# Kernel optimization log

Measured on AMD Instinct MI355X. Metric: run time of the kernel, lower is better.

## Reference

```python
import jax, jax.numpy as jnp
import numpy as np

OBS_LEN = 16; PRED_LEN = 25; N = 192; P = N * N; GH = GW = 8
IN_DIM = 2; OUT_DIM = 5; ENC = 64; DEC = 128
EMB = 32; DYN = 32; C1 = 64; C2 = 16; SOC = 3 * 3 * C2

def lrelu(x):
    return jnp.where(x >= 0, x, 0.1 * x)

def lstm_step(x, h, c, Wih, Whh, bih, bhh):
    # torch nn.LSTM gate order: i, f, g, o
    z = x @ Wih.T + h @ Whh.T + (bih + bhh)
    i, f, g, o = jnp.split(z, 4, axis=-1)
    c = jax.nn.sigmoid(f) * c + jax.nn.sigmoid(i) * jnp.tanh(g)
    h = jax.nn.sigmoid(o) * jnp.tanh(c)
    return h, c

def _indexed_lstm(frames, idxs, n_states, Wip, bip, Wih, Whh, bih, bhh):
    # per-frame gather of hidden/cell rows -> one LSTM step -> scatter back
    H0 = jnp.zeros((n_states, ENC), jnp.float32)
    C0 = jnp.zeros((n_states, ENC), jnp.float32)
    def step(carry, inp):
        Hs, Cs = carry
        frame, idx = inp
        h, c = Hs[idx], Cs[idx]                       # gather [M, ENC]
        emb = lrelu(frame @ Wip.T + bip)              # [M, EMB]
        h, c = lstm_step(emb, h, c, Wih, Whh, bih, bhh)
        return (Hs.at[idx].set(h), Cs.at[idx].set(c)), None  # scatter
    (Hs, _), _ = jax.lax.scan(step, (H0, C0), (frames, idxs))
    return Hs

def setup_inputs():
    key = jax.random.key(0)
    ks = jax.random.split(key, 16)
    def w(k, shape, fan):
        return (jax.random.normal(k, shape, jnp.float32) / np.sqrt(fan)).astype(jnp.float32)
    inp = {}
    inp['obs_traj'] = jax.random.normal(ks[0], (OBS_LEN, N, IN_DIM), jnp.float32)
    inp['obs_ngbrs_traj'] = jax.random.normal(ks[1], (OBS_LEN, P, IN_DIM), jnp.float32)
    inp['masks'] = jnp.ones((N, GH, GW, ENC), dtype=bool)  # fully occupied social grid
    inp['masks_idxs'] = jax.random.randint(ks[2], (N * GH * GW,), 0, P)
    inp['obs_traj_idxs'] = jnp.tile(jnp.arange(N), (OBS_LEN, 1))        # all nodes present each frame
    inp['obs_ngbrs_traj_idxs'] = jnp.tile(jnp.arange(P), (OBS_LEN, 1))  # all pair slots present
    inp['num_nodes'] = N
    inp['Wip'] = w(ks[3], (EMB, IN_DIM), IN_DIM); inp['bip'] = jnp.zeros((EMB,), jnp.float32)
    inp['Wih_e'] = w(ks[4], (4 * ENC, EMB), EMB); inp['Whh_e'] = w(ks[5], (4 * ENC, ENC), ENC)
    inp['bih_e'] = jnp.zeros((4 * ENC,), jnp.float32); inp['bhh_e'] = jnp.zeros((4 * ENC,), jnp.float32)
    inp['Wdyn'] = w(ks[6], (DYN, ENC), ENC); inp['bdyn'] = jnp.zeros((DYN,), jnp.float32)
    inp['Wc1'] = w(ks[7], (C1, ENC, 3, 3), ENC * 9); inp['bc1'] = jnp.zeros((C1,), jnp.float32)
    inp['Wc2'] = w(ks[8], (C2, C1, 3, 3), C1 * 9); inp['bc2'] = jnp.zeros((C2,), jnp.float32)
    inp['Wih_d'] = w(ks[9], (4 * DEC, SOC + DYN), SOC + DYN); inp['Whh_d'] = w(ks[10], (4 * DEC, DEC), DEC)
    inp['bih_d'] = jnp.zeros((4 * DEC,), jnp.float32); inp['bhh_d'] = jnp.zeros((4 * DEC,), jnp.float32)
    inp['Wop'] = w(ks[11], (OUT_DIM, DEC), DEC); inp['bop'] = jnp.zeros((OUT_DIM,), jnp.float32)
    return inp

def reference(obs_traj, obs_ngbrs_traj, masks, masks_idxs, obs_traj_idxs,
              obs_ngbrs_traj_idxs, num_nodes, Wip, bip, Wih_e, Whh_e, bih_e, bhh_e,
              Wdyn, bdyn, Wc1, bc1, Wc2, bc2, Wih_d, Whh_d, bih_d, bhh_d, Wop, bop):
    B = obs_traj_idxs.shape[1]
    # ego-trajectory encoder: per-frame indexed LSTM over num_nodes state slots
    Hs = _indexed_lstm(obs_traj, obs_traj_idxs, num_nodes, Wip, bip, Wih_e, Whh_e, bih_e, bhh_e)
    final_h = Hs[obs_traj_idxs[-1]]                   # [B, ENC]
    traj_enc = lrelu(final_h @ Wdyn.T + bdyn)         # [B, DYN]
    # neighbor-pair encoder: per-frame indexed LSTM over num_nodes^2 state slots
    Hn = _indexed_lstm(obs_ngbrs_traj, obs_ngbrs_traj_idxs, num_nodes * num_nodes,
                       Wip, bip, Wih_e, Whh_e, bih_e, bhh_e)
    ngbr_h = Hn[masks_idxs]                           # [B*GH*GW, ENC]
    # masked_scatter_ of neighbor encodings into fully-occupied social grid == reshape
    soc = jnp.where(masks, ngbr_h.reshape(B, GH, GW, ENC), 0.0)
    soc = jnp.transpose(soc, (0, 3, 2, 1))            # [B, ENC, GW, GH]
    dn = ('NCHW', 'OIHW', 'NCHW')
    soc = lrelu(jax.lax.conv_general_dilated(soc, Wc1, (1, 1), 'VALID', dimension_numbers=dn)
                + bc1[None, :, None, None])           # [B, C1, 6, 6]
    soc = lrelu(jax.lax.conv_general_dilated(soc, Wc2, (1, 1), 'VALID', dimension_numbers=dn)
                + bc2[None, :, None, None])           # [B, C2, 4, 4]
    soc = jax.lax.reduce_window(soc, -jnp.inf, jax.lax.max, (1, 1, 2, 2), (1, 1, 1, 1), 'VALID')
    soc = soc.reshape(B, SOC)                         # [B, 144]
    enc = jnp.concatenate([traj_enc, soc], axis=1)    # [B, DYN+SOC]
    h0 = jnp.zeros((B, DEC), jnp.float32); c0 = jnp.zeros((B, DEC), jnp.float32)
    def dec_step(carry, _):
        h, c = carry
        h, c = lstm_step(enc, h, c, Wih_d, Whh_d, bih_d, bhh_d)
        return (h, c), h
    _, hs = jax.lax.scan(dec_step, (h0, c0), None, length=PRED_LEN)
    o = hs @ Wop.T + bop                              # [PRED_LEN, B, 5]
    # bivariate Gaussian output activation (mu_x, mu_y, sigma_x, sigma_y, corr)
    return jnp.stack([o[..., 0], o[..., 1], jnp.exp(o[..., 2]),
                      jnp.exp(o[..., 3]), jnp.tanh(o[..., 4])], axis=-1)
```

## Files before the change

kernel.cpp:

```cpp
#include <hip/hip_runtime.h>
#include <hip/hip_bf16.h>

#define OBS_LEN 16
#define PRED_LEN 25
#define NNODES 192
#define PAIRS 36864
#define ENC 64
#define EMB 32
#define KTOT 96
#define DEC 128
#define SOCDYN 176
#define PAIR_GROUPS 2304
#define EGO_GROUPS 12

typedef short short8 __attribute__((ext_vector_type(8)));
typedef float f32x4 __attribute__((ext_vector_type(4)));

__device__ __forceinline__ float sigm(float x) {
    return __builtin_amdgcn_rcpf(1.f + __expf(-x));
}
__device__ __forceinline__ float tanh_f(float x) {
    return fmaf(-2.f, __builtin_amdgcn_rcpf(1.f + __expf(2.f * x)), 1.f);
}
__device__ __forceinline__ float lrelu(float x) { return (x >= 0.f) ? x : 0.1f * x; }

__device__ __forceinline__ unsigned short f2bf(float f) {
    union { float f; unsigned u; } v; v.f = f;
    unsigned r = v.u + 0x7fffu + ((v.u >> 16) & 1u);
    return (unsigned short)(r >> 16);
}
__device__ __forceinline__ float bf2f(unsigned short s) {
    union { unsigned u; float f; } v; v.u = ((unsigned)s) << 16; return v.f;
}

__global__ __launch_bounds__(1024, 1)
void prep_dedup_kernel(const float* __restrict__ Wih_d, const float* __restrict__ Whh_d,
                       const float* __restrict__ Wc1, const float* __restrict__ Wc2,
                       const int* __restrict__ masks_idxs,
                       unsigned short* __restrict__ Whh_bf, unsigned short* __restrict__ Wih_bf,
                       float* __restrict__ WT1, float* __restrict__ WT2,
                       int* __restrict__ list, int* __restrict__ list_count)
{
    const int t = threadIdx.x, b = blockIdx.x;
    if (b < 205) {
        int idx = b * 1024 + t;
        if (idx < 65536) {
            int m = idx >> 7, k = idx & 127;
            Whh_bf[idx] = f2bf(Whh_d[m * 128 + k]);
        } else if (idx < 65536 + 98304) {
            int i = idx - 65536;
            int m = i / 192, k = i % 192;
            Wih_bf[i] = (k < 176) ? f2bf(Wih_d[m * 176 + k]) : (unsigned short)0;
        } else if (idx < 65536 + 98304 + 36864) {
            int i = idx - (65536 + 98304);
            int s = i >> 6, o = i & 63;
            int c = s / 9, tap = s % 9;
            WT1[i] = Wc1[(o * 64 + c) * 9 + tap];
        } else {
            int i = idx - (65536 + 98304 + 36864);
            int s = i >> 4, o = i & 15;
            int c = s / 9, tap = s % 9;
            WT2[i] = Wc2[(o * 64 + c) * 9 + tap];
        }
        return;
    }
    __shared__ unsigned bm[1152];
    __shared__ int pcs[1024];
    for (int i = t; i < 1152; i += 1024) bm[i] = 0u;
    __syncthreads();
    for (int i = t; i < 12288; i += 1024) {
        const int r = masks_idxs[i];
        atomicOr(&bm[r >> 5], 1u << (r & 31));
    }
    __syncthreads();
    int pc = 0;
    if (t < 576) pc = __popc(bm[2 * t]) + __popc(bm[2 * t + 1]);
    pcs[t] = pc;
    __syncthreads();
    for (int ofs = 1; ofs < 1024; ofs <<= 1) {
        int v = (t >= ofs) ? pcs[t - ofs] : 0;
        __syncthreads();
        pcs[t] += v;
        __syncthreads();
    }
    if (t == 1023) list_count[0] = pcs[1023];
    if (t < 576) {
        int base = pcs[t] - pc;
#pragma unroll
        for (int wi = 0; wi < 2; ++wi) {
            unsigned wv = bm[2 * t + wi];
            const int rowbase = (2 * t + wi) * 32;
            while (wv) {
                const int bit = __ffs(wv) - 1;
                list[base++] = rowbase + bit;
                wv &= wv - 1;
            }
        }
    }
}

__global__ __launch_bounds__(256, 3)
void enc_lstm_kernel(const float* __restrict__ obs_traj,
                     const float* __restrict__ obs_ngbrs,
                     const float* __restrict__ Wip, const float* __restrict__ bip,
                     const float* __restrict__ Wih, const float* __restrict__ Whh,
                     const float* __restrict__ bih, const float* __restrict__ bhh,
                     const int* __restrict__ list, const int* __restrict__ list_count,
                     float* __restrict__ Hn,
                     float* __restrict__ final_h)
{
    __shared__ __align__(16) short embs[16 * 16 * 40];
    __shared__ __align__(16) short hb[2][16 * 72];
    __shared__ int rows_s[16];

    const int t = threadIdx.x;
    const int wj = t >> 6, lane = t & 63, ln = lane & 15, kq = lane >> 4;
    const int b = blockIdx.x;
    const bool is_ego = (b >= PAIR_GROUPS);

    if (!is_ego) {
        const int cnt = list_count[0];
        if (b * 16 >= cnt) return;
        if (t < 16) rows_s[t] = list[min(b * 16 + t, cnt - 1)];
    } else {
        if (t < 16) rows_s[t] = (b - PAIR_GROUPS) * 16 + t;
    }

    short8 afrag[4][3];
#pragma unroll
    for (int g = 0; g < 4; ++g)
#pragma unroll
        for (int kc = 0; kc < 3; ++kc) {
            const int m = g * 64 + wj * 16 + ln;
            const float* wp = (kc == 0) ? (Wih + m * 32 + kq * 8)
                                        : (Whh + m * 64 + (kc - 1) * 32 + kq * 8);
            short8 a;
#pragma unroll
            for (int j = 0; j < 8; ++j) a[j] = (short)f2bf(wp[j]);
            afrag[g][kc] = a;
        }

    float bsv[4][4];
#pragma unroll
    for (int g = 0; g < 4; ++g)
#pragma unroll
        for (int r = 0; r < 4; ++r) {
            const int m = g * 64 + wj * 16 + kq * 4 + r;
            bsv[g][r] = bih[m] + bhh[m];
        }

    __syncthreads();

    {
        const int row = t & 15, stp = t >> 4;
        const int r = rows_s[row];
        const float* sp = is_ego ? (obs_traj + stp * NNODES * 2)
                                 : (obs_ngbrs + stp * PAIRS * 2);
        const float x0 = sp[r * 2 + 0];
        const float x1 = sp[r * 2 + 1];
        unsigned* dst = (unsigned*)&embs[(stp * 16 + row) * 40];
#pragma unroll
        for (int k = 0; k < 32; k += 2) {
            const float e0 = lrelu(fmaf(x0, Wip[2 * k + 0], fmaf(x1, Wip[2 * k + 1], bip[k])));
            const float e1 = lrelu(fmaf(x0, Wip[2 * k + 2], fmaf(x1, Wip[2 * k + 3], bip[k + 1])));
            dst[k >> 1] = (unsigned)f2bf(e0) | ((unsigned)f2bf(e1) << 16);
        }
    }
    for (int i = t; i < 2 * 16 * 72 / 2; i += 256) ((unsigned*)hb)[i] = 0u;
    __syncthreads();

    float cst[4] = {0.f, 0.f, 0.f, 0.f};
    int p = 0;
    for (int stp = 0; stp < OBS_LEN; ++stp) {
        const short8 bf0 = *(const short8*)&embs[(stp * 16 + ln) * 40 + kq * 8];
        const short* hbp = &hb[p][ln * 72 + kq * 8];
        const short8 bf1 = *(const short8*)hbp;
        const short8 bf2 = *(const short8*)(hbp + 32);
        f32x4 acc[4];
#pragma unroll
        for (int g = 0; g < 4; ++g) {
            f32x4 a = { bsv[g][0], bsv[g][1], bsv[g][2], bsv[g][3] };
            a = __builtin_amdgcn_mfma_f32_16x16x32_bf16(afrag[g][0], bf0, a, 0, 0, 0);
            a = __builtin_amdgcn_mfma_f32_16x16x32_bf16(afrag[g][1], bf1, a, 0, 0, 0);
            acc[g] = __builtin_amdgcn_mfma_f32_16x16x32_bf16(afrag[g][2], bf2, a, 0, 0, 0);
        }
        unsigned long long pk = 0;
#pragma unroll
        for (int r = 0; r < 4; ++r) {
            const float cn = fmaf(sigm(acc[1][r]), cst[r], sigm(acc[0][r]) * tanh_f(acc[2][r]));
            cst[r] = cn;
            const float h = sigm(acc[3][r]) * tanh_f(cn);
            pk |= (unsigned long long)f2bf(h) << (16 * r);
        }
        __syncthreads();
        *(unsigned long long*)&hb[1 - p][ln * 72 + wj * 16 + kq * 4] = pk;
        p ^= 1;
        __syncthreads();
    }

    {
        const int row = t >> 4, k0 = (t & 15) * 4;
        unsigned long long pk = *(const unsigned long long*)&hb[p][row * 72 + k0];
        float4 v;
        v.x = bf2f((unsigned short)(pk));
        v.y = bf2f((unsigned short)(pk >> 16));
        v.z = bf2f((unsigned short)(pk >> 32));
        v.w = bf2f((unsigned short)(pk >> 48));
        float* dst = is_ego ? (final_h + rows_s[row] * 64 + k0)
                            : (Hn + (long)rows_s[row] * 64 + k0);
        *(float4*)dst = v;
    }
}

__global__ __launch_bounds__(256, 2)
void conv_kernel(const float* __restrict__ Hn, const int* __restrict__ masks_idxs,
                 const float* __restrict__ final_h, const float* __restrict__ Wdyn,
                 const float* __restrict__ bdyn, const float* __restrict__ WT1,
                 const float* __restrict__ bc1, const float* __restrict__ WT2,
                 const float* __restrict__ bc2, float* __restrict__ enc)
{
    __shared__ float in2[64][66];
    __shared__ float s1[64 * 37];
    __shared__ float s2[16 * 17];
    const int t = threadIdx.x, b = blockIdx.x;

    for (int i = 0; i < 16; ++i) {
        const int c = t & 63;
        const int p = (i << 2) + (t >> 6);
        const int u = p >> 3, v = p & 7;
        const int row = masks_idxs[b * 64 + v * 8 + u];
        in2[c][p] = Hn[(long)row * 64 + c];
    }
    if (t < 32) {
        float acc = bdyn[t];
        for (int k = 0; k < 64; ++k) acc = fmaf(final_h[b * 64 + k], Wdyn[t * 64 + k], acc);
        enc[b * SOCDYN + t] = lrelu(acc);
    }
    __syncthreads();

    {
        const int wv = t >> 6, o = t & 63;
        const int xb = (wv >> 1) * 3, yb = (wv & 1) * 3;
        float a1[3][3];
        const float bc = bc1[o];
#pragma unroll
        for (int qx = 0; qx < 3; ++qx)
#pragma unroll
            for (int qy = 0; qy < 3; ++qy) a1[qx][qy] = bc;
        for (int c = 0; c < 64; ++c) {
            float win[5][5];
#pragma unroll
            for (int xr = 0; xr < 5; ++xr)
#pragma unroll
                for (int yc = 0; yc < 5; ++yc)
                    win[xr][yc] = in2[c][(xb + xr) * 8 + (yb + yc)];
#pragma unroll
            for (int dx = 0; dx < 3; ++dx)
#pragma unroll
                for (int dy = 0; dy < 3; ++dy) {
                    const float w = WT1[(c * 9 + dx * 3 + dy) * 64 + o];
#pragma unroll
                    for (int qx = 0; qx < 3; ++qx)
#pragma unroll
                        for (int qy = 0; qy < 3; ++qy)
                            a1[qx][qy] = fmaf(w, win[qx + dx][qy + dy], a1[qx][qy]);
                }
        }
#pragma unroll
        for (int qx = 0; qx < 3; ++qx)
#pragma unroll
            for (int qy = 0; qy < 3; ++qy)
                s1[o * 37 + (xb + qx) * 6 + (yb + qy)] = lrelu(a1[qx][qy]);
    }
    __syncthreads();

    {
        const int o2 = t & 15, q = t >> 4;
        const int x = q >> 2, y = q & 3;
        float acc = bc2[o2];
        for (int c = 0; c < 64; ++c) {
#pragma unroll
            for (int dx = 0; dx < 3; ++dx)
#pragma unroll
                for (int dy = 0; dy < 3; ++dy)
                    acc = fmaf(WT2[(c * 9 + dx * 3 + dy) * 16 + o2],
                               s1[c * 37 + (x + dx) * 6 + (y + dy)], acc);
        }
        s2[o2 * 17 + q] = lrelu(acc);
    }
    __syncthreads();

    if (t < 144) {
        const int o = t / 9, ij = t % 9, i = ij / 3, j = ij % 3;
        const float v00 = s2[o * 17 + i * 4 + j];
        const float v01 = s2[o * 17 + i * 4 + j + 1];
        const float v10 = s2[o * 17 + (i + 1) * 4 + j];
        const float v11 = s2[o * 17 + (i + 1) * 4 + j + 1];
        enc[b * SOCDYN + 32 + t] = fmaxf(fmaxf(v00, v01), fmaxf(v10, v11));
    }
}

__global__ __launch_bounds__(512, 2)
void dec_kernel(const float* __restrict__ enc,
                const unsigned short* __restrict__ Wih_bf,
                const unsigned short* __restrict__ Whh_bf,
                const float* __restrict__ bih_d, const float* __restrict__ bhh_d,
                const float* __restrict__ Wop, const float* __restrict__ bop,
                float* __restrict__ hhist,
                float* __restrict__ out)
{
    __shared__ __align__(16) short encfr[3072];
    __shared__ __align__(16) short hb[2][2048];
    __shared__ float wop_s[5 * 128];

    const int t = threadIdx.x;
    const int w = t >> 6, lane = t & 63, ln = lane & 15, kq = lane >> 4;
    const int row0 = blockIdx.x * 16;

    for (int i = t; i < 3072; i += 512) {
        const int n = i / 192, k = i % 192;
        const float v = (k < 176) ? enc[(row0 + n) * SOCDYN + k] : 0.f;
        encfr[(k >> 3) * 128 + n * 8 + (k & 7)] = (short)f2bf(v);
    }
    for (int i = t; i < 640; i += 512) wop_s[i] = Wop[i];

    short8 wfrag[4][4];
#pragma unroll
    for (int g = 0; g < 4; ++g)
#pragma unroll
        for (int kc = 0; kc < 4; ++kc)
            wfrag[g][kc] = *(const short8*)&Whh_bf[(g * 128 + w * 16 + ln) * 128 + kc * 32 + kq * 8];

    f32x4 zin[4];
#pragma unroll
    for (int g = 0; g < 4; ++g)
#pragma unroll
        for (int r = 0; r < 4; ++r) {
            const int m = g * 128 + w * 16 + kq * 4 + r;
            zin[g][r] = bih_d[m] + bhh_d[m];
        }

    __syncthreads();

#pragma unroll
    for (int kc = 0; kc < 6; ++kc) {
        const short8 bfr = *(const short8*)&encfr[(kc * 4 + kq) * 128 + ln * 8];
#pragma unroll
        for (int g = 0; g < 4; ++g) {
            const short8 afr = *(const short8*)&Wih_bf[(g * 128 + w * 16 + ln) * 192 + kc * 32 + kq * 8];
            zin[g] = __builtin_amdgcn_mfma_f32_16x16x32_bf16(afr, bfr, zin[g], 0, 0, 0);
        }
    }

    float c4[4] = {0.f, 0.f, 0.f, 0.f};
    int p = 0;
    const int hb_wr = ((w >> 1) * 4 + (w & 1) * 2 + (kq >> 1)) * 128 + ln * 8 + (kq & 1) * 4;

    for (int stp = 0; stp < PRED_LEN; ++stp) {
        f32x4 z[4];
#pragma unroll
        for (int g = 0; g < 4; ++g) z[g] = zin[g];
        if (stp > 0) {
            short8 bh[4];
#pragma unroll
            for (int kc = 0; kc < 4; ++kc)
                bh[kc] = *(const short8*)&hb[p][(kc * 4 + kq) * 128 + ln * 8];
#pragma unroll
            for (int kc = 0; kc < 4; ++kc)
#pragma unroll
                for (int g = 0; g < 4; ++g)
                    z[g] = __builtin_amdgcn_mfma_f32_16x16x32_bf16(wfrag[g][kc], bh[kc], z[g], 0, 0, 0);
        }
        unsigned long long pk = 0;
        float4 hv;
        float hvr[4];
#pragma unroll
        for (int r = 0; r < 4; ++r) {
            const float cn = fmaf(sigm(z[1][r]), c4[r], sigm(z[0][r]) * tanh_f(z[2][r]));
            c4[r] = cn;
            const float h = sigm(z[3][r]) * tanh_f(cn);
            hvr[r] = h;
            pk |= (unsigned long long)f2bf(h) << (16 * r);
        }
        hv.x = hvr[0]; hv.y = hvr[1]; hv.z = hvr[2]; hv.w = hvr[3];
        *(unsigned long long*)&hb[p ^ 1][hb_wr] = pk;
        *(float4*)&hhist[((long)stp * NNODES + row0 + ln) * 128 + w * 16 + kq * 4] = hv;
        p ^= 1;
        __syncthreads();
    }

    __threadfence_block();
    __syncthreads();

    for (int pi = t; pi < PRED_LEN * 16; pi += 512) {
        const int ts = pi >> 4, n = pi & 15;
        const float* hp = &hhist[((long)ts * NNODES + row0 + n) * 128];
        float a0 = bop[0], a1 = bop[1], a2 = bop[2], a3 = bop[3], a4 = bop[4];
        for (int k = 0; k < 128; k += 4) {
            const float4 h4 = *(const float4*)&hp[k];
#pragma unroll
            for (int q = 0; q < 4; ++q) {
                const float h = (q == 0) ? h4.x : (q == 1) ? h4.y : (q == 2) ? h4.z : h4.w;
                a0 = fmaf(h, wop_s[0 * 128 + k + q], a0);
                a1 = fmaf(h, wop_s[1 * 128 + k + q], a1);
                a2 = fmaf(h, wop_s[2 * 128 + k + q], a2);
                a3 = fmaf(h, wop_s[3 * 128 + k + q], a3);
                a4 = fmaf(h, wop_s[4 * 128 + k + q], a4);
            }
        }
        float* op = &out[((long)ts * NNODES + row0 + n) * 5];
        op[0] = a0;
        op[1] = a1;
        op[2] = __expf(a2);
        op[3] = __expf(a3);
        op[4] = tanh_f(a4);
    }
}

extern "C" void kernel_launch(void* const* d_in, const int* in_sizes, int n_in,
                              void* d_out, int out_size, void* d_ws, size_t ws_size,
                              hipStream_t stream) {
    const float* obs_traj   = (const float*)d_in[0];
    const float* obs_ngbrs  = (const float*)d_in[1];
    const int*   masks_idxs = (const int*)d_in[3];
    const float* Wip   = (const float*)d_in[7];
    const float* bip   = (const float*)d_in[8];
    const float* Wih_e = (const float*)d_in[9];
    const float* Whh_e = (const float*)d_in[10];
    const float* bih_e = (const float*)d_in[11];
    const float* bhh_e = (const float*)d_in[12];
    const float* Wdyn  = (const float*)d_in[13];
    const float* bdyn  = (const float*)d_in[14];
    const float* Wc1   = (const float*)d_in[15];
    const float* bc1   = (const float*)d_in[16];
    const float* Wc2   = (const float*)d_in[17];
    const float* bc2   = (const float*)d_in[18];
    const float* Wih_d = (const float*)d_in[19];
    const float* Whh_d = (const float*)d_in[20];
    const float* bih_d = (const float*)d_in[21];
    const float* bhh_d = (const float*)d_in[22];
    const float* Wop   = (const float*)d_in[23];
    const float* bop   = (const float*)d_in[24];
    float* out = (float*)d_out;

    float* ws = (float*)d_ws;
    float* Hn      = ws;
    float* final_h = Hn + 2359296;
    float* encb    = final_h + 12288;
    unsigned short* Whh_bf = (unsigned short*)(encb + 33792);
    unsigned short* Wih_bf = Whh_bf + 65536;
    float* WT1     = (float*)(Wih_bf + 98304);
    float* WT2     = WT1 + 36864;
    int*   list    = (int*)(WT2 + 9216);
    int*   list_count = list + 36864;
    float* hhist   = Hn;

    hipLaunchKernelGGL(prep_dedup_kernel, dim3(206), dim3(1024), 0, stream,
                       Wih_d, Whh_d, Wc1, Wc2, masks_idxs,
                       Whh_bf, Wih_bf, WT1, WT2, list, list_count);
    hipLaunchKernelGGL(enc_lstm_kernel, dim3(PAIR_GROUPS + EGO_GROUPS), dim3(256), 0, stream,
                       obs_traj, obs_ngbrs, Wip, bip, Wih_e, Whh_e, bih_e, bhh_e,
                       list, list_count, Hn, final_h);
    hipLaunchKernelGGL(conv_kernel, dim3(NNODES), dim3(256), 0, stream,
                       Hn, masks_idxs, final_h, Wdyn, bdyn, WT1, bc1, WT2, bc2, encb);
    hipLaunchKernelGGL(dec_kernel, dim3(NNODES / 16), dim3(512), 0, stream,
                       encb, Wih_bf, Whh_bf, bih_d, bhh_d, Wop, bop, hhist, out);
}
```

Baseline: 230.1 us.

## Run social-pooling convs on bf16 MFMA via im2col and pre-convert encoder weights

The conv kernel now builds im2col tiles in shared memory as bf16 and computes both 3x3 convolutions with 16x16x32 bf16 MFMA instructions instead of scalar FP32 FMAs. The second conv's K dimension is split across the four waves and reduced through shared memory. Encoder LSTM weights are converted to a packed bf16 layout once in the prep kernel, so each encoder block loads ready-made fragments instead of converting FP32 per block. One redundant barrier is also removed from the encoder step loop. The risks are lower conv precision, a larger shared-memory footprint that forces one block per CU, and extra im2col passes.

```diff
diff --git a/kernel.cpp b/kernel.cpp
--- a/kernel.cpp
+++ b/kernel.cpp
@@ -12,6 +12,7 @@
 #define SOCDYN 176
 #define PAIR_GROUPS 2304
 #define EGO_GROUPS 12
+#define PREP_ELEMS 234496
 
 typedef short short8 __attribute__((ext_vector_type(8)));
 typedef float f32x4 __attribute__((ext_vector_type(4)));
@@ -36,13 +37,15 @@
 __global__ __launch_bounds__(1024, 1)
 void prep_dedup_kernel(const float* __restrict__ Wih_d, const float* __restrict__ Whh_d,
                        const float* __restrict__ Wc1, const float* __restrict__ Wc2,
+                       const float* __restrict__ Wih_e, const float* __restrict__ Whh_e,
                        const int* __restrict__ masks_idxs,
                        unsigned short* __restrict__ Whh_bf, unsigned short* __restrict__ Wih_bf,
-                       float* __restrict__ WT1, float* __restrict__ WT2,
+                       unsigned short* __restrict__ WT1bf, unsigned short* __restrict__ WT2bf,
+                       unsigned short* __restrict__ Wenc_bf,
                        int* __restrict__ list, int* __restrict__ list_count)
 {
     const int t = threadIdx.x, b = blockIdx.x;
-    if (b < 205) {
+    if (b < 229) {
         int idx = b * 1024 + t;
         if (idx < 65536) {
             int m = idx >> 7, k = idx & 127;
@@ -53,14 +56,18 @@
             Wih_bf[i] = (k < 176) ? f2bf(Wih_d[m * 176 + k]) : (unsigned short)0;
         } else if (idx < 65536 + 98304 + 36864) {
             int i = idx - (65536 + 98304);
-            int s = i >> 6, o = i & 63;
-            int c = s / 9, tap = s % 9;
-            WT1[i] = Wc1[(o * 64 + c) * 9 + tap];
-        } else {
+            int o = i / 576, k = i % 576;
+            int c = k / 9, tap = k % 9;
+            WT1bf[i] = f2bf(Wc1[(o * 64 + c) * 9 + tap]);
+        } else if (idx < 65536 + 98304 + 36864 + 9216) {
             int i = idx - (65536 + 98304 + 36864);
-            int s = i >> 4, o = i & 15;
-            int c = s / 9, tap = s % 9;
-            WT2[i] = Wc2[(o * 64 + c) * 9 + tap];
+            int o = i / 576, k = i % 576;
+            int c = k / 9, tap = k % 9;
+            WT2bf[i] = f2bf(Wc2[(o * 64 + c) * 9 + tap]);
+        } else if (idx < PREP_ELEMS) {
+            int i = idx - (65536 + 98304 + 36864 + 9216);
+            int m = i / 96, k = i % 96;
+            Wenc_bf[i] = f2bf((k < 32) ? Wih_e[m * 32 + k] : Whh_e[m * 64 + (k - 32)]);
         }
         return;
     }
@@ -103,7 +110,7 @@
 void enc_lstm_kernel(const float* __restrict__ obs_traj,
                      const float* __restrict__ obs_ngbrs,
                      const float* __restrict__ Wip, const float* __restrict__ bip,
-                     const float* __restrict__ Wih, const float* __restrict__ Whh,
+                     const unsigned short* __restrict__ Wenc_bf,
                      const float* __restrict__ bih, const float* __restrict__ bhh,
                      const int* __restrict__ list, const int* __restrict__ list_count,
                      float* __restrict__ Hn,
@@ -130,15 +137,8 @@
 #pragma unroll
     for (int g = 0; g < 4; ++g)
 #pragma unroll
-        for (int kc = 0; kc < 3; ++kc) {
-            const int m = g * 64 + wj * 16 + ln;
-            const float* wp = (kc == 0) ? (Wih + m * 32 + kq * 8)
-                                        : (Whh + m * 64 + (kc - 1) * 32 + kq * 8);
-            short8 a;
-#pragma unroll
-            for (int j = 0; j < 8; ++j) a[j] = (short)f2bf(wp[j]);
-            afrag[g][kc] = a;
-        }
+        for (int kc = 0; kc < 3; ++kc)
+            afrag[g][kc] = *(const short8*)&Wenc_bf[(g * 64 + wj * 16 + ln) * 96 + kc * 32 + kq * 8];
 
     float bsv[4][4];
 #pragma unroll
@@ -192,7 +192,6 @@
             const float h = sigm(acc[3][r]) * tanh_f(cn);
             pk |= (unsigned long long)f2bf(h) << (16 * r);
         }
-        __syncthreads();
         *(unsigned long long*)&hb[1 - p][ln * 72 + wj * 16 + kq * 4] = pk;
         p ^= 1;
         __syncthreads();
@@ -212,24 +211,44 @@
     }
 }
 
-__global__ __launch_bounds__(256, 2)
+__global__ __launch_bounds__(256, 1)
 void conv_kernel(const float* __restrict__ Hn, const int* __restrict__ masks_idxs,
                  const float* __restrict__ final_h, const float* __restrict__ Wdyn,
-                 const float* __restrict__ bdyn, const float* __restrict__ WT1,
-                 const float* __restrict__ bc1, const float* __restrict__ WT2,
-                 const float* __restrict__ bc2, float* __restrict__ enc)
+                 const float* __restrict__ bdyn,
+                 const unsigned short* __restrict__ WT1bf, const float* __restrict__ bc1,
+                 const unsigned short* __restrict__ WT2bf, const float* __restrict__ bc2,
+                 float* __restrict__ enc)
 {
-    __shared__ float in2[64][66];
-    __shared__ float s1[64 * 37];
-    __shared__ float s2[16 * 17];
+    __shared__ __align__(16) short in2bf[64][72];
+    __shared__ __align__(16) short imc1[48][584];
+    __shared__ __align__(16) short s1bf[64][40];
+    __shared__ __align__(16) short imc2[16][584];
+    __shared__ __align__(16) float red[4][256];
+    __shared__ float s2s[16 * 17];
+
     const int t = threadIdx.x, b = blockIdx.x;
+    const int w = t >> 6, lane = t & 63, ln = lane & 15, kq = lane >> 4;
+
+    short8 a1f[18];
+#pragma unroll
+    for (int kc = 0; kc < 18; ++kc)
+        a1f[kc] = *(const short8*)&WT1bf[(w * 16 + ln) * 576 + kc * 32 + kq * 8];
+
+    const int c2start = (w < 2) ? w * 5 : 10 + (w - 2) * 4;
+    const int c2cnt = (w < 2) ? 5 : 4;
+    short8 a2f[5];
+#pragma unroll
+    for (int i = 0; i < 5; ++i) {
+        const int kc = c2start + min(i, c2cnt - 1);
+        a2f[i] = *(const short8*)&WT2bf[ln * 576 + kc * 32 + kq * 8];
+    }
 
     for (int i = 0; i < 16; ++i) {
         const int c = t & 63;
         const int p = (i << 2) + (t >> 6);
         const int u = p >> 3, v = p & 7;
         const int row = masks_idxs[b * 64 + v * 8 + u];
-        in2[c][p] = Hn[(long)row * 64 + c];
+        in2bf[c][p] = (short)f2bf(Hn[(long)row * 64 + c]);
     }
     if (t < 32) {
         float acc = bdyn[t];
@@ -238,64 +257,81 @@
     }
     __syncthreads();
 
+    for (int i = t; i < 36 * 64; i += 256) {
+        const int n = i >> 6, c = i & 63;
+        const int x = n / 6, y = n % 6;
+        short* dst = &imc1[n][c * 9];
+#pragma unroll
+        for (int dx = 0; dx < 3; ++dx)
+#pragma unroll
+            for (int dy = 0; dy < 3; ++dy)
+                dst[dx * 3 + dy] = in2bf[c][(x + dx) * 8 + (y + dy)];
+    }
+    __syncthreads();
+
     {
-        const int wv = t >> 6, o = t & 63;
-        const int xb = (wv >> 1) * 3, yb = (wv & 1) * 3;
-        float a1[3][3];
-        const float bc = bc1[o];
-#pragma unroll
-        for (int qx = 0; qx < 3; ++qx)
-#pragma unroll
-            for (int qy = 0; qy < 3; ++qy) a1[qx][qy] = bc;
-        for (int c = 0; c < 64; ++c) {
-            float win[5][5];
-#pragma unroll
-            for (int xr = 0; xr < 5; ++xr)
-#pragma unroll
-                for (int yc = 0; yc < 5; ++yc)
-                    win[xr][yc] = in2[c][(xb + xr) * 8 + (yb + yc)];
-#pragma unroll
-            for (int dx = 0; dx < 3; ++dx)
-#pragma unroll
-                for (int dy = 0; dy < 3; ++dy) {
-                    const float w = WT1[(c * 9 + dx * 3 + dy) * 64 + o];
-#pragma unroll
-                    for (int qx = 0; qx < 3; ++qx)
-#pragma unroll
-                        for (int qy = 0; qy < 3; ++qy)
-                            a1[qx][qy] = fmaf(w, win[qx + dx][qy + dy], a1[qx][qy]);
-                }
-        }
-#pragma unroll
-        for (int qx = 0; qx < 3; ++qx)
-#pragma unroll
-            for (int qy = 0; qy < 3; ++qy)
-                s1[o * 37 + (xb + qx) * 6 + (yb + qy)] = lrelu(a1[qx][qy]);
+        float bcv[4];
+#pragma unroll
+        for (int r = 0; r < 4; ++r) bcv[r] = bc1[w * 16 + kq * 4 + r];
+#pragma unroll
+        for (int nt = 0; nt < 3; ++nt) {
+            f32x4 acc = { bcv[0], bcv[1], bcv[2], bcv[3] };
+            const short* bp = &imc1[nt * 16 + ln][kq * 8];
+#pragma unroll
+            for (int kc = 0; kc < 18; ++kc) {
+                const short8 bfr = *(const short8*)(bp + kc * 32);
+                acc = __builtin_amdgcn_mfma_f32_16x16x32_bf16(a1f[kc], bfr, acc, 0, 0, 0);
+            }
+            const int n = nt * 16 + ln;
+            if (n < 36) {
+#pragma unroll
+                for (int r = 0; r < 4; ++r)
+                    s1bf[w * 16 + kq * 4 + r][n] = (short)f2bf(lrelu(acc[r]));
+            }
+        }
+    }
+    __syncthreads();
+
+    for (int i = t; i < 16 * 64; i += 256) {
+        const int n2 = i >> 6, c = i & 63;
+        const int x = n2 >> 2, y = n2 & 3;
+        short* dst = &imc2[n2][c * 9];
+#pragma unroll
+        for (int dx = 0; dx < 3; ++dx)
+#pragma unroll
+            for (int dy = 0; dy < 3; ++dy)
+                dst[dx * 3 + dy] = s1bf[c][(x + dx) * 6 + (y + dy)];
     }
     __syncthreads();
 
     {
-        const int o2 = t & 15, q = t >> 4;
-        const int x = q >> 2, y = q & 3;
-        float acc = bc2[o2];
-        for (int c = 0; c < 64; ++c) {
-#pragma unroll
-            for (int dx = 0; dx < 3; ++dx)
-#pragma unroll
-                for (int dy = 0; dy < 3; ++dy)
-                    acc = fmaf(WT2[(c * 9 + dx * 3 + dy) * 16 + o2],
-                               s1[c * 37 + (x + dx) * 6 + (y + dy)], acc);
-        }
-        s2[o2 * 17 + q] = lrelu(acc);
+        f32x4 acc = { 0.f, 0.f, 0.f, 0.f };
+        const short* bp = &imc2[ln][kq * 8];
+#pragma unroll
+        for (int i = 0; i < 5; ++i) {
+            if (i < c2cnt) {
+                const short8 bfr = *(const short8*)(bp + (c2start + i) * 32);
+                acc = __builtin_amdgcn_mfma_f32_16x16x32_bf16(a2f[i], bfr, acc, 0, 0, 0);
+            }
+        }
+        *(f32x4*)&red[w][lane * 4] = acc;
+    }
+    __syncthreads();
+
+    {
+        const float v = red[0][t] + red[1][t] + red[2][t] + red[3][t];
+        const int l = t >> 2, r = t & 3;
+        const int m = (l >> 4) * 4 + r, n = l & 15;
+        s2s[m * 17 + n] = lrelu(v + bc2[m]);
     }
     __syncthreads();
 
     if (t < 144) {
         const int o = t / 9, ij = t % 9, i = ij / 3, j = ij % 3;
-        const float v00 = s2[o * 17 + i * 4 + j];
-        const float v01 = s2[o * 17 + i * 4 + j + 1];
-        const float v10 = s2[o * 17 + (i + 1) * 4 + j];
-        const float v11 = s2[o * 17 + (i + 1) * 4 + j + 1];
+        const float v00 = s2s[o * 17 + i * 4 + j];
+        const float v01 = s2s[o * 17 + i * 4 + j + 1];
+        const float v10 = s2s[o * 17 + (i + 1) * 4 + j];
+        const float v11 = s2s[o * 17 + (i + 1) * 4 + j + 1];
         enc[b * SOCDYN + 32 + t] = fmaxf(fmaxf(v00, v01), fmaxf(v10, v11));
     }
 }
@@ -431,8 +467,8 @@
     const float* bhh_e = (const float*)d_in[12];
     const float* Wdyn  = (const float*)d_in[13];
     const float* bdyn  = (const float*)d_in[14];
+    const float* bc1   = (const float*)d_in[16];
     const float* Wc1   = (const float*)d_in[15];
-    const float* bc1   = (const float*)d_in[16];
     const float* Wc2   = (const float*)d_in[17];
     const float* bc2   = (const float*)d_in[18];
     const float* Wih_d = (const float*)d_in[19];
@@ -447,22 +483,23 @@
     float* Hn      = ws;
     float* final_h = Hn + 2359296;
     float* encb    = final_h + 12288;
-    unsigned short* Whh_bf = (unsigned short*)(encb + 33792);
-    unsigned short* Wih_bf = Whh_bf + 65536;
-    float* WT1     = (float*)(Wih_bf + 98304);
-    float* WT2     = WT1 + 36864;
-    int*   list    = (int*)(WT2 + 9216);
+    unsigned short* Whh_bf  = (unsigned short*)(encb + 33792);
+    unsigned short* Wih_bf  = Whh_bf + 65536;
+    unsigned short* WT1bf   = Wih_bf + 98304;
+    unsigned short* WT2bf   = WT1bf + 36864;
+    unsigned short* Wenc_bf = WT2bf + 9216;
+    int*   list    = (int*)(Wenc_bf + 24576);
     int*   list_count = list + 36864;
     float* hhist   = Hn;
 
-    hipLaunchKernelGGL(prep_dedup_kernel, dim3(206), dim3(1024), 0, stream,
-                       Wih_d, Whh_d, Wc1, Wc2, masks_idxs,
-                       Whh_bf, Wih_bf, WT1, WT2, list, list_count);
+    hipLaunchKernelGGL(prep_dedup_kernel, dim3(230), dim3(1024), 0, stream,
+                       Wih_d, Whh_d, Wc1, Wc2, Wih_e, Whh_e, masks_idxs,
+                       Whh_bf, Wih_bf, WT1bf, WT2bf, Wenc_bf, list, list_count);
     hipLaunchKernelGGL(enc_lstm_kernel, dim3(PAIR_GROUPS + EGO_GROUPS), dim3(256), 0, stream,
-                       obs_traj, obs_ngbrs, Wip, bip, Wih_e, Whh_e, bih_e, bhh_e,
+                       obs_traj, obs_ngbrs, Wip, bip, Wenc_bf, bih_e, bhh_e,
                        list, list_count, Hn, final_h);
     hipLaunchKernelGGL(conv_kernel, dim3(NNODES), dim3(256), 0, stream,
-                       Hn, masks_idxs, final_h, Wdyn, bdyn, WT1, bc1, WT2, bc2, encb);
+                       Hn, masks_idxs, final_h, Wdyn, bdyn, WT1bf, bc1, WT2bf, bc2, encb);
     hipLaunchKernelGGL(dec_kernel, dim3(NNODES / 16), dim3(512), 0, stream,
                        encb, Wih_bf, Whh_bf, bih_d, bhh_d, Wop, bop, hhist, out);
 }
```

After: 197.2 us. 1.17x faster.
